# Performance work log

Hardware: AMD Instinct MI355X
Metric: run time of the kernel (lower is better)

## Reference

```python
import jax, jax.numpy as jnp
import numpy as np

QMAX = 7.0  # 4-bit symmetric: levels in [-8, 7]

def quant4(w):
    # per-tensor symmetric 4-bit fake-quant with straight-through estimator
    s = jnp.max(jnp.abs(w)) / QMAX
    q = jnp.clip(jnp.round(w / s), -8.0, 7.0) * s
    return w + jax.lax.stop_gradient(q - w)

def setup_inputs() -> dict:
    key = jax.random.key(0)
    ks = jax.random.split(key, 7)
    B = 2048
    x = jax.random.normal(ks[0], (B, 1, 31, 16, 31), dtype=jnp.float32)
    # conv: out_ch=1, in_ch=1, kernel (5,3,5)
    w_conv = jax.random.normal(ks[1], (1, 1, 5, 3, 5), dtype=jnp.float32) * 0.1
    b_conv = jax.random.normal(ks[2], (1,), dtype=jnp.float32) * 0.1
    w_fc1 = jax.random.normal(ks[3], (128, 343), dtype=jnp.float32) * 0.05
    b_fc1 = jax.random.normal(ks[4], (128,), dtype=jnp.float32) * 0.05
    w_fc2 = jax.random.normal(ks[5], (4, 128), dtype=jnp.float32) * 0.05
    b_fc2 = jax.random.normal(ks[6], (4,), dtype=jnp.float32) * 0.05
    return {"x": x, "w_conv": w_conv, "b_conv": b_conv,
            "w_fc1": w_fc1, "b_fc1": b_fc1, "w_fc2": w_fc2, "b_fc2": b_fc2}

def reference(x, w_conv, b_conv, w_fc1, b_fc1, w_fc2, b_fc2):
    # QuantConv3d: 4-bit quantized weights, stride (2,1,2), no padding
    c1 = jax.lax.conv_general_dilated(
        x, quant4(w_conv), window_strides=(2, 1, 2), padding='VALID',
        dimension_numbers=('NCDHW', 'OIDHW', 'NCDHW'))
    c1 = c1 + b_conv.reshape(1, -1, 1, 1, 1)          # [B,1,14,14,14]
    # MaxPool3d(2)
    p1 = jax.lax.reduce_window(c1, -jnp.inf, jax.lax.max,
                               (1, 1, 2, 2, 2), (1, 1, 2, 2, 2), 'VALID')  # [B,1,7,7,7]
    f = p1.reshape(p1.shape[0], -1)                   # [B,343]
    a1 = jax.nn.relu(f @ quant4(w_fc1).T + b_fc1)     # [B,128]
    s2 = a1 @ quant4(w_fc2).T + b_fc2                 # [B,4]
    return jax.nn.softmax(s2, axis=1)
```

## Files before the change

kernel.cpp:

```cpp
#include <hip/hip_runtime.h>
#include <hip/hip_bf16.h>

#define WS_PARTIAL 0
#define WS_WCONV   128
#define WS_W1T     256
#define WS_W2      44160
#define WS_FEAT    45056

__global__ __launch_bounds__(256) void quant_reduce(
    const float* __restrict__ wconv, const float* __restrict__ w1,
    const float* __restrict__ w2, float* __restrict__ ws) {
  __shared__ float red[256];
  int b = blockIdx.x, t = threadIdx.x;
  float m = 0.f;
  if (b < 64) {
    int base = b * 686;
    for (int i = t; i < 686; i += 256) m = fmaxf(m, fabsf(w1[base + i]));
  } else if (b == 64) {
    for (int i = t; i < 75; i += 256) m = fmaxf(m, fabsf(wconv[i]));
  } else {
    for (int i = t; i < 512; i += 256) m = fmaxf(m, fabsf(w2[i]));
  }
  red[t] = m;
  __syncthreads();
  for (int s = 128; s > 0; s >>= 1) {
    if (t < s) red[t] = fmaxf(red[t], red[t + s]);
    __syncthreads();
  }
  if (t == 0) ws[WS_PARTIAL + b] = red[0];
}

__device__ __forceinline__ float q4(float w, float s) {
  if (s <= 0.f) return 0.f;
  float r = rintf(w / s);
  r = fminf(fmaxf(r, -8.f), 7.f);
  return r * s;
}

__global__ __launch_bounds__(256) void quant_write(
    const float* __restrict__ wconv, const float* __restrict__ w1,
    const float* __restrict__ w2, float* __restrict__ ws) {
  int b = blockIdx.x, t = threadIdx.x;
  __shared__ float sSs;
  if (b < 86) {
    float m = (t < 64) ? ws[WS_PARTIAL + t] : 0.f;
    #pragma unroll
    for (int off = 32; off; off >>= 1) m = fmaxf(m, __shfl_down(m, off));
    if (t == 0) sSs = m * (1.0f / 7.0f);
    __syncthreads();
    float s = sSs;
    #pragma unroll
    for (int k = 0; k < 2; ++k) {
      int idx = b * 512 + k * 256 + t;
      if (idx < 43904) {
        float q = q4(w1[idx], s);
        int o = idx / 343;
        int j = idx - o * 343;
        ws[WS_W1T + j * 128 + o] = q;
      }
    }
  } else if (b == 86) {
    float s = ws[WS_PARTIAL + 64] * (1.0f / 7.0f);
    if (t < 75) ws[WS_WCONV + t] = q4(wconv[t], s);
  } else {
    float s = ws[WS_PARTIAL + 65] * (1.0f / 7.0f);
    #pragma unroll
    for (int k = 0; k < 2; ++k) {
      int idx = k * 256 + t;
      ws[WS_W2 + idx] = q4(w2[idx], s);
    }
  }
}

__global__ __launch_bounds__(256, 4) void conv_pool(
    const float* __restrict__ x, const float* __restrict__ bconv,
    const float* __restrict__ ws, float* __restrict__ feat) {
  __shared__ float xs[9500];
  int t = threadIdx.x;
  int half = blockIdx.x & 1;
  int b = blockIdx.x >> 1;
  int d0 = half ? 16 : 0;
  int nfl4 = half ? 1860 : 2356;

  const float4* src = (const float4*)(x + (size_t)b * 15376 + d0 * 496);
  for (int i = t; i < nfl4; i += 256) {
    float4 v = src[i];
    int gi = i * 4;
    int d = gi / 496;
    int rem = gi - d * 496;
    *(float4*)&xs[d * 500 + rem] = v;
  }
  __syncthreads();

  int npf = half ? 147 : 196;
  if (t < npf) {
    int pdl = t / 49;
    int rr = t - pdl * 49;
    int ph = rr / 7;
    int pw = rr - ph * 7;
    const float* wq = ws + WS_WCONV;
    float c[8];
    #pragma unroll
    for (int i = 0; i < 8; ++i) c[i] = 0.f;

    #pragma unroll
    for (int dd = 0; dd < 7; ++dd) {
      float rg[4][7];
      const float* p = &xs[(4 * pdl + dd) * 500 + (2 * ph) * 31 + 4 * pw];
      #pragma unroll
      for (int hh = 0; hh < 4; ++hh)
        #pragma unroll
        for (int ww = 0; ww < 7; ++ww)
          rg[hh][ww] = p[hh * 31 + ww];
      #pragma unroll
      for (int odp = 0; odp < 2; ++odp) {
        int kd = dd - 2 * odp;
        if (kd < 0 || kd >= 5) continue;
        #pragma unroll
        for (int ohp = 0; ohp < 2; ++ohp)
          #pragma unroll
          for (int owp = 0; owp < 2; ++owp) {
            float a = c[odp * 4 + ohp * 2 + owp];
            #pragma unroll
            for (int kh = 0; kh < 3; ++kh)
              #pragma unroll
              for (int kw = 0; kw < 5; ++kw)
                a = fmaf(rg[ohp + kh][2 * owp + kw],
                         wq[kd * 15 + kh * 5 + kw], a);
            c[odp * 4 + ohp * 2 + owp] = a;
          }
      }
    }
    float m = c[0];
    #pragma unroll
    for (int i = 1; i < 8; ++i) m = fmaxf(m, c[i]);
    int pd = pdl + (half ? 4 : 0);
    feat[b * 343 + pd * 49 + rr] = m + bconv[0];
  }
}

__global__ __launch_bounds__(256) void fc_head(
    const float* __restrict__ ws, const float* __restrict__ bfc1,
    const float* __restrict__ bfc2, float* __restrict__ out) {
  __shared__ float fs[1372];
  __shared__ float fc1p[4][128];
  __shared__ float a1s[4][128];
  __shared__ float s2[16];
  int t = threadIdx.x;
  int b0 = blockIdx.x * 4;

  const float4* fsrc = (const float4*)(ws + WS_FEAT + (size_t)b0 * 343);
  for (int i = t; i < 343; i += 256) ((float4*)fs)[i] = fsrc[i];
  __syncthreads();

  int g = t >> 7, o = t & 127;
  const float* w1T = ws + WS_W1T;
  float acc0 = 0.f, acc1 = 0.f, acc2 = 0.f, acc3 = 0.f;
  int j0 = g ? 172 : 0;
  int j1 = g ? 343 : 172;
  for (int j = j0; j < j1; ++j) {
    float w = w1T[j * 128 + o];
    acc0 = fmaf(fs[j], w, acc0);
    acc1 = fmaf(fs[343 + j], w, acc1);
    acc2 = fmaf(fs[686 + j], w, acc2);
    acc3 = fmaf(fs[1029 + j], w, acc3);
  }
  if (g) {
    fc1p[0][o] = acc0; fc1p[1][o] = acc1;
    fc1p[2][o] = acc2; fc1p[3][o] = acc3;
  }
  __syncthreads();
  if (!g) {
    float bo = bfc1[o];
    a1s[0][o] = fmaxf(acc0 + fc1p[0][o] + bo, 0.f);
    a1s[1][o] = fmaxf(acc1 + fc1p[1][o] + bo, 0.f);
    a1s[2][o] = fmaxf(acc2 + fc1p[2][o] + bo, 0.f);
    a1s[3][o] = fmaxf(acc3 + fc1p[3][o] + bo, 0.f);
  }
  __syncthreads();
  if (t < 16) {
    int bb = t >> 2, cls = t & 3;
    const float* w2 = ws + WS_W2 + cls * 128;
    float a = bfc2[cls];
    for (int k = 0; k < 128; ++k) a = fmaf(a1s[bb][k], w2[k], a);
    s2[t] = a;
  }
  __syncthreads();
  if (t < 16) {
    int bb = t >> 2, cls = t & 3;
    float v0 = s2[bb * 4], v1 = s2[bb * 4 + 1];
    float v2 = s2[bb * 4 + 2], v3 = s2[bb * 4 + 3];
    float m = fmaxf(fmaxf(v0, v1), fmaxf(v2, v3));
    float e0 = expf(v0 - m), e1 = expf(v1 - m);
    float e2 = expf(v2 - m), e3 = expf(v3 - m);
    float inv = 1.f / (e0 + e1 + e2 + e3);
    float mine = (cls == 0) ? e0 : (cls == 1) ? e1 : (cls == 2) ? e2 : e3;
    out[(b0 + bb) * 4 + cls] = mine * inv;
  }
}

extern "C" void kernel_launch(void* const* d_in, const int* in_sizes, int n_in,
                              void* d_out, int out_size, void* d_ws, size_t ws_size,
                              hipStream_t stream) {
  const float* x     = (const float*)d_in[0];
  const float* wconv = (const float*)d_in[1];
  const float* bconv = (const float*)d_in[2];
  const float* wfc1  = (const float*)d_in[3];
  const float* bfc1  = (const float*)d_in[4];
  const float* wfc2  = (const float*)d_in[5];
  const float* bfc2  = (const float*)d_in[6];
  float* out = (float*)d_out;
  float* ws  = (float*)d_ws;

  quant_reduce<<<66, 256, 0, stream>>>(wconv, wfc1, wfc2, ws);
  quant_write<<<88, 256, 0, stream>>>(wconv, wfc1, wfc2, ws);
  conv_pool<<<4096, 256, 0, stream>>>(x, bconv, ws, ws + WS_FEAT);
  fc_head<<<512, 256, 0, stream>>>(ws, bfc1, bfc2, out);
}
```

Before: 258.6 us.

## Fuse weight quant kernels, compact conv smem copy, batch 8 rows in fc head

Merges the two weight-quantization kernels into one, so each fc1 block recomputes the global max itself rather than reading partials from a separate launch. The conv kernel now copies input to shared memory contiguously without per-slice padding, and its loop is restructured to load one row at a time to cut register pressure. The fc head handles 8 batch rows per block instead of 4, halving the block count and reusing each weight load across more rows. Risks include redundant max reductions across 88 blocks and possible bank conflicts from the removed padding.

```diff
diff --git a/kernel.cpp b/kernel.cpp
--- a/kernel.cpp
+++ b/kernel.cpp
@@ -1,34 +1,10 @@
 #include <hip/hip_runtime.h>
 #include <hip/hip_bf16.h>
 
-#define WS_PARTIAL 0
 #define WS_WCONV   128
 #define WS_W1T     256
 #define WS_W2      44160
 #define WS_FEAT    45056
-
-__global__ __launch_bounds__(256) void quant_reduce(
-    const float* __restrict__ wconv, const float* __restrict__ w1,
-    const float* __restrict__ w2, float* __restrict__ ws) {
-  __shared__ float red[256];
-  int b = blockIdx.x, t = threadIdx.x;
-  float m = 0.f;
-  if (b < 64) {
-    int base = b * 686;
-    for (int i = t; i < 686; i += 256) m = fmaxf(m, fabsf(w1[base + i]));
-  } else if (b == 64) {
-    for (int i = t; i < 75; i += 256) m = fmaxf(m, fabsf(wconv[i]));
-  } else {
-    for (int i = t; i < 512; i += 256) m = fmaxf(m, fabsf(w2[i]));
-  }
-  red[t] = m;
-  __syncthreads();
-  for (int s = 128; s > 0; s >>= 1) {
-    if (t < s) red[t] = fmaxf(red[t], red[t + s]);
-    __syncthreads();
-  }
-  if (t == 0) ws[WS_PARTIAL + b] = red[0];
-}
 
 __device__ __forceinline__ float q4(float w, float s) {
   if (s <= 0.f) return 0.f;
@@ -37,18 +13,26 @@
   return r * s;
 }
 
-__global__ __launch_bounds__(256) void quant_write(
+__global__ __launch_bounds__(256) void quant_all(
     const float* __restrict__ wconv, const float* __restrict__ w1,
     const float* __restrict__ w2, float* __restrict__ ws) {
+  __shared__ float red[256];
   int b = blockIdx.x, t = threadIdx.x;
-  __shared__ float sSs;
-  if (b < 86) {
-    float m = (t < 64) ? ws[WS_PARTIAL + t] : 0.f;
-    #pragma unroll
-    for (int off = 32; off; off >>= 1) m = fmaxf(m, __shfl_down(m, off));
-    if (t == 0) sSs = m * (1.0f / 7.0f);
-    __syncthreads();
-    float s = sSs;
+  if (b < 88) {
+    const float4* w4 = (const float4*)w1;
+    float m = 0.f;
+    for (int i = t; i < 10976; i += 256) {
+      float4 v = w4[i];
+      m = fmaxf(m, fmaxf(fmaxf(fabsf(v.x), fabsf(v.y)),
+                         fmaxf(fabsf(v.z), fabsf(v.w))));
+    }
+    red[t] = m;
+    __syncthreads();
+    for (int s = 128; s > 0; s >>= 1) {
+      if (t < s) red[t] = fmaxf(red[t], red[t + s]);
+      __syncthreads();
+    }
+    float s = red[0] * (1.0f / 7.0f);
     #pragma unroll
     for (int k = 0; k < 2; ++k) {
       int idx = b * 512 + k * 256 + t;
@@ -59,15 +43,30 @@
         ws[WS_W1T + j * 128 + o] = q;
       }
     }
-  } else if (b == 86) {
-    float s = ws[WS_PARTIAL + 64] * (1.0f / 7.0f);
-    if (t < 75) ws[WS_WCONV + t] = q4(wconv[t], s);
   } else {
-    float s = ws[WS_PARTIAL + 65] * (1.0f / 7.0f);
+    float mc = (t < 75) ? fabsf(wconv[t]) : 0.f;
+    float m2 = 0.f;
+    for (int i = t; i < 512; i += 256) m2 = fmaxf(m2, fabsf(w2[i]));
+    red[t] = mc;
+    __syncthreads();
+    for (int s = 128; s > 0; s >>= 1) {
+      if (t < s) red[t] = fmaxf(red[t], red[t + s]);
+      __syncthreads();
+    }
+    float sc = red[0] * (1.0f / 7.0f);
+    __syncthreads();
+    red[t] = m2;
+    __syncthreads();
+    for (int s = 128; s > 0; s >>= 1) {
+      if (t < s) red[t] = fmaxf(red[t], red[t + s]);
+      __syncthreads();
+    }
+    float s2 = red[0] * (1.0f / 7.0f);
+    if (t < 75) ws[WS_WCONV + t] = q4(wconv[t], sc);
     #pragma unroll
     for (int k = 0; k < 2; ++k) {
       int idx = k * 256 + t;
-      ws[WS_W2 + idx] = q4(w2[idx], s);
+      ws[WS_W2 + idx] = q4(w2[idx], s2);
     }
   }
 }
@@ -75,7 +74,7 @@
 __global__ __launch_bounds__(256, 4) void conv_pool(
     const float* __restrict__ x, const float* __restrict__ bconv,
     const float* __restrict__ ws, float* __restrict__ feat) {
-  __shared__ float xs[9500];
+  __shared__ float xs[9424];
   int t = threadIdx.x;
   int half = blockIdx.x & 1;
   int b = blockIdx.x >> 1;
@@ -83,57 +82,53 @@
   int nfl4 = half ? 1860 : 2356;
 
   const float4* src = (const float4*)(x + (size_t)b * 15376 + d0 * 496);
-  for (int i = t; i < nfl4; i += 256) {
-    float4 v = src[i];
-    int gi = i * 4;
-    int d = gi / 496;
-    int rem = gi - d * 496;
-    *(float4*)&xs[d * 500 + rem] = v;
-  }
+  float4* dst = (float4*)xs;
+  for (int i = t; i < nfl4; i += 256) dst[i] = src[i];
   __syncthreads();
 
   int npf = half ? 147 : 196;
   if (t < npf) {
     int pdl = t / 49;
-    int rr = t - pdl * 49;
-    int ph = rr / 7;
-    int pw = rr - ph * 7;
+    int rr  = t - pdl * 49;
+    int ph  = rr / 7;
+    int pw  = rr - ph * 7;
     const float* wq = ws + WS_WCONV;
-    float c[8];
-    #pragma unroll
-    for (int i = 0; i < 8; ++i) c[i] = 0.f;
-
+    float c[2][2][2];
+    #pragma unroll
+    for (int i = 0; i < 8; ++i) ((float*)c)[i] = 0.f;
+
+    int base0 = pdl * (4 * 496) + ph * 62 + pw * 4;
     #pragma unroll
     for (int dd = 0; dd < 7; ++dd) {
-      float rg[4][7];
-      const float* p = &xs[(4 * pdl + dd) * 500 + (2 * ph) * 31 + 4 * pw];
+      int rbase = base0 + dd * 496;
       #pragma unroll
-      for (int hh = 0; hh < 4; ++hh)
+      for (int hh = 0; hh < 4; ++hh) {
+        float row[7];
         #pragma unroll
-        for (int ww = 0; ww < 7; ++ww)
-          rg[hh][ww] = p[hh * 31 + ww];
-      #pragma unroll
-      for (int odp = 0; odp < 2; ++odp) {
-        int kd = dd - 2 * odp;
-        if (kd < 0 || kd >= 5) continue;
+        for (int wi = 0; wi < 7; ++wi) row[wi] = xs[rbase + hh * 31 + wi];
         #pragma unroll
-        for (int ohp = 0; ohp < 2; ++ohp)
+        for (int odp = 0; odp < 2; ++odp) {
+          int kd = dd - 2 * odp;
+          if (kd < 0 || kd > 4) continue;
           #pragma unroll
-          for (int owp = 0; owp < 2; ++owp) {
-            float a = c[odp * 4 + ohp * 2 + owp];
+          for (int ohp = 0; ohp < 2; ++ohp) {
+            int kh = hh - ohp;
+            if (kh < 0 || kh > 2) continue;
             #pragma unroll
-            for (int kh = 0; kh < 3; ++kh)
+            for (int owp = 0; owp < 2; ++owp) {
+              float a = c[odp][ohp][owp];
               #pragma unroll
               for (int kw = 0; kw < 5; ++kw)
-                a = fmaf(rg[ohp + kh][2 * owp + kw],
-                         wq[kd * 15 + kh * 5 + kw], a);
-            c[odp * 4 + ohp * 2 + owp] = a;
+                a = fmaf(row[2 * owp + kw], wq[kd * 15 + kh * 5 + kw], a);
+              c[odp][ohp][owp] = a;
+            }
           }
+        }
       }
     }
-    float m = c[0];
-    #pragma unroll
-    for (int i = 1; i < 8; ++i) m = fmaxf(m, c[i]);
+    float m = ((float*)c)[0];
+    #pragma unroll
+    for (int i = 1; i < 8; ++i) m = fmaxf(m, ((float*)c)[i]);
     int pd = pdl + (half ? 4 : 0);
     feat[b * 343 + pd * 49 + rr] = m + bconv[0];
   }
@@ -142,43 +137,43 @@
 __global__ __launch_bounds__(256) void fc_head(
     const float* __restrict__ ws, const float* __restrict__ bfc1,
     const float* __restrict__ bfc2, float* __restrict__ out) {
-  __shared__ float fs[1372];
-  __shared__ float fc1p[4][128];
-  __shared__ float a1s[4][128];
-  __shared__ float s2[16];
+  __shared__ float fs[2744];
+  __shared__ float fc1p[8][128];
+  __shared__ float a1s[8][132];
+  __shared__ float s2[32];
   int t = threadIdx.x;
-  int b0 = blockIdx.x * 4;
+  int b0 = blockIdx.x * 8;
 
   const float4* fsrc = (const float4*)(ws + WS_FEAT + (size_t)b0 * 343);
-  for (int i = t; i < 343; i += 256) ((float4*)fs)[i] = fsrc[i];
+  for (int i = t; i < 686; i += 256) ((float4*)fs)[i] = fsrc[i];
   __syncthreads();
 
   int g = t >> 7, o = t & 127;
   const float* w1T = ws + WS_W1T;
-  float acc0 = 0.f, acc1 = 0.f, acc2 = 0.f, acc3 = 0.f;
+  float acc[8];
+  #pragma unroll
+  for (int i = 0; i < 8; ++i) acc[i] = 0.f;
   int j0 = g ? 172 : 0;
   int j1 = g ? 343 : 172;
   for (int j = j0; j < j1; ++j) {
     float w = w1T[j * 128 + o];
-    acc0 = fmaf(fs[j], w, acc0);
-    acc1 = fmaf(fs[343 + j], w, acc1);
-    acc2 = fmaf(fs[686 + j], w, acc2);
-    acc3 = fmaf(fs[1029 + j], w, acc3);
+    #pragma unroll
+    for (int bi = 0; bi < 8; ++bi)
+      acc[bi] = fmaf(fs[bi * 343 + j], w, acc[bi]);
   }
   if (g) {
-    fc1p[0][o] = acc0; fc1p[1][o] = acc1;
-    fc1p[2][o] = acc2; fc1p[3][o] = acc3;
+    #pragma unroll
+    for (int bi = 0; bi < 8; ++bi) fc1p[bi][o] = acc[bi];
   }
   __syncthreads();
   if (!g) {
     float bo = bfc1[o];
-    a1s[0][o] = fmaxf(acc0 + fc1p[0][o] + bo, 0.f);
-    a1s[1][o] = fmaxf(acc1 + fc1p[1][o] + bo, 0.f);
-    a1s[2][o] = fmaxf(acc2 + fc1p[2][o] + bo, 0.f);
-    a1s[3][o] = fmaxf(acc3 + fc1p[3][o] + bo, 0.f);
-  }
-  __syncthreads();
-  if (t < 16) {
+    #pragma unroll
+    for (int bi = 0; bi < 8; ++bi)
+      a1s[bi][o] = fmaxf(acc[bi] + fc1p[bi][o] + bo, 0.f);
+  }
+  __syncthreads();
+  if (t < 32) {
     int bb = t >> 2, cls = t & 3;
     const float* w2 = ws + WS_W2 + cls * 128;
     float a = bfc2[cls];
@@ -186,7 +181,7 @@
     s2[t] = a;
   }
   __syncthreads();
-  if (t < 16) {
+  if (t < 32) {
     int bb = t >> 2, cls = t & 3;
     float v0 = s2[bb * 4], v1 = s2[bb * 4 + 1];
     float v2 = s2[bb * 4 + 2], v3 = s2[bb * 4 + 3];
@@ -212,8 +207,7 @@
   float* out = (float*)d_out;
   float* ws  = (float*)d_ws;
 
-  quant_reduce<<<66, 256, 0, stream>>>(wconv, wfc1, wfc2, ws);
-  quant_write<<<88, 256, 0, stream>>>(wconv, wfc1, wfc2, ws);
+  quant_all<<<89, 256, 0, stream>>>(wconv, wfc1, wfc2, ws);
   conv_pool<<<4096, 256, 0, stream>>>(x, bconv, ws, ws + WS_FEAT);
-  fc_head<<<512, 256, 0, stream>>>(ws, bfc1, bfc2, out);
-}
+  fc_head<<<256, 256, 0, stream>>>(ws, bfc1, bfc2, out);
+}
```

New measurement: 266.0 us. 2.9% more time.
